# Optimization experiments

Hardware: AMD Instinct MI355X
Metric: run time of the kernel (lower is better)

Reference implementation:

```python
import jax, jax.numpy as jnp
import numpy as np

B, T, D = 64, 2048, 64
M_DIM = 8            # pthdv_m
N_GROUPS = 4         # out_dim // m^2 * 4
GD = D // N_GROUPS   # 16, per-group channel dim
OUT_DIM = 64
SE_HID = OUT_DIM // 16  # reduction ratio 16 -> 4


def expm(A):
    """Batched matrix exponential via fixed scaling-and-squaring + Taylor-12.
    A: (..., m, m) with modest norm (skew-symmetric from small weights)."""
    s = 6
    A = A * (1.0 / (2 ** s))
    eye = jnp.eye(A.shape[-1], dtype=A.dtype)
    term = jnp.broadcast_to(eye, A.shape)
    out = term
    for k in range(1, 13):
        term = jnp.matmul(term, A) / k
        out = out + term
    for _ in range(s):
        out = jnp.matmul(out, out)
    return out


def layernorm(x, g, b, eps=1e-5):
    mu = jnp.mean(x, axis=-1, keepdims=True)
    var = jnp.var(x, axis=-1, keepdims=True)
    return (x - mu) * jax.lax.rsqrt(var + eps) * g + b


def lin_interp(f, t_out):
    """F.interpolate(mode='linear', align_corners=False) along axis 1. f: (B,L,C)."""
    L = f.shape[1]
    pos = (jnp.arange(t_out, dtype=f.dtype) + 0.5) * (L / t_out) - 0.5
    pos = jnp.clip(pos, 0.0, L - 1.0)
    i0 = jnp.floor(pos).astype(jnp.int32)
    i1 = jnp.minimum(i0 + 1, L - 1)
    w = (pos - i0.astype(f.dtype))[None, :, None]
    return f[:, i0] * (1.0 - w) + f[:, i1] * w


def setup_inputs() -> dict:
    key = jax.random.key(0)
    ks = jax.random.split(key, 8)
    x = jax.random.normal(ks[0], (B, T, D), dtype=jnp.float32)
    mask = jnp.ones((B, T), dtype=jnp.float32)
    W_dev = jax.random.normal(ks[1], (N_GROUPS, GD, M_DIM, M_DIM), dtype=jnp.float32) * 0.1
    ln_gamma = jnp.ones((M_DIM * M_DIM,), dtype=jnp.float32)
    ln_beta = jnp.zeros((M_DIM * M_DIM,), dtype=jnp.float32)
    cf = N_GROUPS * M_DIM * M_DIM  # 256
    proj_w = jax.random.normal(ks[2], (cf, OUT_DIM), dtype=jnp.float32) / np.sqrt(cf)
    proj_b = jnp.zeros((OUT_DIM,), dtype=jnp.float32)
    se_w1 = jax.random.normal(ks[3], (OUT_DIM, SE_HID), dtype=jnp.float32) / np.sqrt(OUT_DIM)
    se_b1 = jnp.zeros((SE_HID,), dtype=jnp.float32)
    se_w2 = jax.random.normal(ks[4], (SE_HID, OUT_DIM), dtype=jnp.float32) / np.sqrt(SE_HID)
    se_b2 = jnp.zeros((OUT_DIM,), dtype=jnp.float32)
    return {"x": x, "mask": mask, "W_dev": W_dev, "ln_gamma": ln_gamma, "ln_beta": ln_beta,
            "proj_w": proj_w, "proj_b": proj_b, "se_w1": se_w1, "se_b1": se_b1,
            "se_w2": se_w2, "se_b2": se_b2}


def reference(x, mask, W_dev, ln_gamma, ln_beta, proj_w, proj_b, se_w1, se_b1, se_w2, se_b2):
    Bc, Tc, Dc = x.shape
    # skew-symmetric (so(m)) projection of raw dev weights: (G, gd, m, m)
    Wl = jnp.tril(W_dev, k=-1)
    S = Wl - jnp.swapaxes(Wl, -1, -2)
    # grouped increments: (B, T-1, G, gd), masked
    xg = x.reshape(Bc, Tc, N_GROUPS, GD)
    dX = (xg[:, 1:] - xg[:, :-1]) * mask[:, 1:, None, None]
    # project increments to Lie algebra: (B, T', G, m, m)
    Mlie = jnp.einsum('btgd,gdij->btgij', dX, S)
    E = expm(Mlie)                                   # path development per window (kernel=2)
    f = E.reshape(Bc, Tc - 1, N_GROUPS, M_DIM * M_DIM)
    f = layernorm(f, ln_gamma, ln_beta)              # shared LN over m^2, per group
    f = f.reshape(Bc, Tc - 1, N_GROUPS * M_DIM * M_DIM)
    f = f @ proj_w + proj_b                          # (B, T-1, out_dim)
    f = lin_interp(f, Tc)                            # back to length T (stride=1)
    h = x + f
    # Squeeze-and-Excitation with masked average pooling
    denom = jnp.sum(mask, axis=1, keepdims=True)     # (B,1)
    pooled = jnp.sum(h * mask[:, :, None], axis=1) / denom  # (B, D)
    s = jax.nn.sigmoid(jax.nn.gelu(pooled @ se_w1 + se_b1, approximate=False) @ se_w2 + se_b2)
    h = h * s[:, None, :]
    out = h + x                                      # res_con is Identity (in_dim==out_dim, stride==1)
    return (out, mask)
```

## Files before the change

kernel.cpp:

```cpp
#include <hip/hip_runtime.h>

#define B_   64
#define T_   2048
#define TM1  2047
#define D_   64

#define PID(i,j) ((i)*((i)-1)/2 + (j))

typedef __attribute__((ext_vector_type(8))) short bf16x8;
typedef __attribute__((ext_vector_type(4))) float f32x4;

__device__ __forceinline__ unsigned f2bf(float v) {
    unsigned u = __float_as_uint(v);
    u = (u + 0x7FFFu + ((u >> 16) & 1u)) >> 16;
    return u;
}
__device__ __forceinline__ float bf2f(unsigned s) {
    return __uint_as_float(s << 16);
}

__global__ void k_prep(const float* __restrict__ pw, unsigned short* __restrict__ pwB)
{
    int idx = blockIdx.x * 256 + threadIdx.x;
    int j  = idx & 7;
    int l  = (idx >> 3) & 63;
    int ks = (idx >> 9) & 7;
    int nt = idx >> 12;
    int k  = ks * 32 + ((l >> 4) << 3) + j;
    int o  = nt * 16 + (l & 15);
    pwB[idx] = (unsigned short)f2bf(pw[k * 64 + o]);
}

__global__ __launch_bounds__(256, 3) void k_expm_f2(
    const float* __restrict__ x, const float* __restrict__ mask,
    const float* __restrict__ Wd, const float* __restrict__ lng,
    const float* __restrict__ lnb, const unsigned short* __restrict__ pwB,
    const float* __restrict__ pb, unsigned short* __restrict__ fbf,
    float* __restrict__ pooled, float* __restrict__ denom)
{
    __shared__ __align__(16) unsigned char smem[32768];
    float* xT = (float*)smem;

    const int tid  = threadIdx.x;
    const int lane = tid & 63;
    const int wq   = __builtin_amdgcn_readfirstlane(tid >> 6);
    const int bl   = blockIdx.x >> 5;
    const int t0   = (blockIdx.x & 31) << 6;

    const float* xb = x + (size_t)bl * (T_ * D_);
    for (int idx = tid; idx < 65 * 64; idx += 256) {
        int r = idx >> 6, c = idx & 63;
        int tr = t0 + r;
        xT[c * 65 + r] = (tr < T_) ? xb[tr * 64 + c] : 0.f;
    }
    __syncthreads();

    const int t = t0 + lane;
    const bool valid = (t < TM1);
    const float* mrow = mask + bl * T_;
    const float mk = valid ? mrow[t + 1] : 0.f;

    {
        const int c  = tid & 63;
        const int rg = tid >> 6;
        float psum = 0.f;
        #pragma unroll
        for (int i = 0; i < 16; ++i) {
            int r = rg * 16 + i;
            psum = fmaf(xT[c * 65 + r], mrow[t0 + r], psum);
        }
        atomicAdd(&pooled[bl * 64 + c], psum);
        if (wq == 0) {
            float dv = mrow[t0 + lane];
            #pragma unroll
            for (int off = 32; off >= 1; off >>= 1) dv += __shfl_xor(dv, off);
            if (lane == 0) atomicAdd(&denom[bl], dv);
        }
    }

    float al[28];
    #pragma unroll
    for (int p = 0; p < 28; ++p) al[p] = 0.f;
    const float* Wg = Wd + wq * (16 * 64);
    #pragma unroll
    for (int d = 0; d < 16; ++d) {
        const float* col = &xT[(wq * 16 + d) * 65 + lane];
        float dxd = (col[1] - col[0]) * mk;
        const float* Wrow = Wg + d * 64;
        #pragma unroll
        for (int i = 1; i < 8; ++i)
            #pragma unroll
            for (int j = 0; j < i; ++j)
                al[PID(i, j)] = fmaf(dxd, Wrow[i * 8 + j], al[PID(i, j)]);
    }
    __syncthreads();

    #pragma unroll
    for (int p = 0; p < 28; ++p) al[p] *= 0.0625f;

    float R[64];
    #pragma unroll
    for (int i = 0; i < 8; ++i)
        #pragma unroll
        for (int j = 0; j < 8; ++j)
            R[i * 8 + j] = (i == j) ? 1.f : 0.f;
    for (int k = 6; k >= 1; --k) {
        float invk = 1.f / (float)k;
        #pragma unroll
        for (int j = 0; j < 8; ++j) {
            float tmp[8];
            #pragma unroll
            for (int i = 0; i < 8; ++i) tmp[i] = R[i * 8 + j];
            #pragma unroll
            for (int i = 0; i < 8; ++i) {
                float s = 0.f;
                #pragma unroll
                for (int kk = 0; kk < 8; ++kk) {
                    if (kk == i) continue;
                    float a = (i > kk) ? al[PID(i, kk)] : -al[PID(kk, i)];
                    s = fmaf(a, tmp[kk], s);
                }
                R[i * 8 + j] = ((i == j) ? 1.f : 0.f) + invk * s;
            }
        }
    }
    for (int sq = 0; sq < 4; ++sq) {
        float nw[64];
        #pragma unroll
        for (int i = 0; i < 8; ++i)
            #pragma unroll
            for (int j = 0; j < 8; ++j) {
                float s = 0.f;
                #pragma unroll
                for (int kk = 0; kk < 8; ++kk)
                    s = fmaf(R[i * 8 + kk], R[kk * 8 + j], s);
                nw[i * 8 + j] = s;
            }
        #pragma unroll
        for (int e = 0; e < 64; ++e) R[e] = nw[e];
    }

    float sum = 0.f, ssq = 0.f;
    #pragma unroll
    for (int e = 0; e < 64; ++e) { sum += R[e]; ssq = fmaf(R[e], R[e], ssq); }
    float mu   = sum * (1.f / 64.f);
    float var  = ssq * (1.f / 64.f) - mu * mu;
    float rstd = rsqrtf(var + 1e-5f);

    #pragma unroll
    for (int eq = 0; eq < 16; ++eq) {
        int e = eq * 4;
        float v0 = fmaf((R[e]   - mu) * rstd, lng[e],   lnb[e]);
        float v1 = fmaf((R[e+1] - mu) * rstd, lng[e+1], lnb[e+1]);
        float v2 = fmaf((R[e+2] - mu) * rstd, lng[e+2], lnb[e+2]);
        float v3 = fmaf((R[e+3] - mu) * rstd, lng[e+3], lnb[e+3]);
        uint2 pk = make_uint2(f2bf(v0) | (f2bf(v1) << 16), f2bf(v2) | (f2bf(v3) << 16));
        int slot = wq * 16 + eq;
        int sw = slot ^ ((lane & 7) << 1);
        *(uint2*)(smem + lane * 512 + sw * 8) = pk;
    }
    __syncthreads();

    f32x4 acc[4];
    #pragma unroll
    for (int nt = 0; nt < 4; ++nt) acc[nt] = (f32x4)(0.f);
    const int arow = wq * 16 + (lane & 15);
    #pragma unroll
    for (int ks = 0; ks < 8; ++ks) {
        int c = ks * 4 + (lane >> 4);
        bf16x8 a = *(const bf16x8*)(smem + arow * 512 + (c ^ (arow & 7)) * 16);
        #pragma unroll
        for (int nt = 0; nt < 4; ++nt) {
            bf16x8 bb = *(const bf16x8*)(pwB + (((nt * 8 + ks) * 64 + lane) << 3));
            acc[nt] = __builtin_amdgcn_mfma_f32_16x16x32_bf16(a, bb, acc[nt], 0, 0, 0);
        }
    }
    __syncthreads();

    unsigned short* fosh = (unsigned short*)smem;
    float bias[4];
    #pragma unroll
    for (int nt = 0; nt < 4; ++nt) bias[nt] = pb[nt * 16 + (lane & 15)];
    float pf[4] = {0.f, 0.f, 0.f, 0.f};
    #pragma unroll
    for (int r = 0; r < 4; ++r) {
        int pl = wq * 16 + ((lane >> 4) << 2) + r;
        int p  = t0 + pl;
        float g = 0.f;
        if (p < TM1) {
            float mp  = mrow[p];
            float mp1 = mrow[p + 1];
            float wlo = (p + 1.5f) * (1.f / 2048.f);
            float whi = 1.f - (p + 0.5f) * (1.f / 2048.f);
            if (p == 0)          g = mp + mp1 * wlo;
            else if (p == 2046)  g = mp * whi + mp1;
            else                 g = mp * whi + mp1 * wlo;
        }
        #pragma unroll
        for (int nt = 0; nt < 4; ++nt) {
            float fv = acc[nt][r] + bias[nt];
            pf[nt] = fmaf(g, fv, pf[nt]);
            fosh[pl * 64 + nt * 16 + (lane & 15)] = (unsigned short)f2bf(fv);
        }
    }
    #pragma unroll
    for (int nt = 0; nt < 4; ++nt) {
        pf[nt] += __shfl_xor(pf[nt], 16);
        pf[nt] += __shfl_xor(pf[nt], 32);
    }
    if (lane < 16) {
        #pragma unroll
        for (int nt = 0; nt < 4; ++nt)
            atomicAdd(&pooled[bl * 64 + nt * 16 + lane], pf[nt]);
    }
    __syncthreads();

    #pragma unroll
    for (int i = 0; i < 2; ++i) {
        int C = i * 256 + tid;
        int row = C >> 3, c = C & 7;
        int p = t0 + row;
        if (p < TM1) {
            uint4 vv = *(const uint4*)(smem + C * 16);
            *(uint4*)(fbf + ((size_t)bl * TM1 + p) * 64 + c * 8) = vv;
        }
    }
}

__global__ void k_se(const float* __restrict__ pooled, const float* __restrict__ denom,
                     const float* __restrict__ w1, const float* __restrict__ b1,
                     const float* __restrict__ w2, const float* __restrict__ b2,
                     float* __restrict__ s_out)
{
    __shared__ float pl[64];
    __shared__ float hid[4];
    const int b = blockIdx.x, o = threadIdx.x;
    float p = pooled[b * 64 + o] / denom[b];
    pl[o] = p;
    __syncthreads();
    if (o < 4) {
        float h = b1[o];
        for (int e = 0; e < 64; ++e) h = fmaf(pl[e], w1[e * 4 + o], h);
        hid[o] = 0.5f * h * (1.f + erff(h * 0.70710678118654752f));
    }
    __syncthreads();
    float sv = b2[o];
    #pragma unroll
    for (int hh = 0; hh < 4; ++hh) sv = fmaf(hid[hh], w2[hh * 64 + o], sv);
    s_out[b * 64 + o] = 1.f / (1.f + expf(-sv));
}

__global__ void k_apply(const float* __restrict__ x, const unsigned short* __restrict__ fbf,
                        const float* __restrict__ s, float* __restrict__ out)
{
    int gid = blockIdx.x * 256 + threadIdx.x;
    int o4 = (gid & 15) << 2;
    int t  = (gid >> 4) & 2047;
    int b  = gid >> 15;
    float pos = fminf(fmaxf((t + 0.5f) * (2047.f / 2048.f) - 0.5f, 0.f), 2046.f);
    int   i0  = (int)pos;
    float w   = pos - (float)i0;
    int   i1  = min(i0 + 1, 2046);
    const unsigned short* fb = fbf + (size_t)b * (TM1 * 64);
    uint2 u0 = *(const uint2*)(fb + i0 * 64 + o4);
    uint2 u1 = *(const uint2*)(fb + i1 * 64 + o4);
    size_t base = ((size_t)b * T_ + t) * 64 + o4;
    float4 xv = *(const float4*)(x + base);
    float4 sv = *(const float4*)(s + b * 64 + o4);
    float4 ov;
    float f00 = bf2f(u0.x & 0xffffu), f01 = bf2f(u0.x >> 16);
    float f02 = bf2f(u0.y & 0xffffu), f03 = bf2f(u0.y >> 16);
    float f10 = bf2f(u1.x & 0xffffu), f11 = bf2f(u1.x >> 16);
    float f12 = bf2f(u1.y & 0xffffu), f13 = bf2f(u1.y >> 16);
    ov.x = fmaf(xv.x + f00 * (1.f - w) + f10 * w, sv.x, xv.x);
    ov.y = fmaf(xv.y + f01 * (1.f - w) + f11 * w, sv.y, xv.y);
    ov.z = fmaf(xv.z + f02 * (1.f - w) + f12 * w, sv.z, xv.z);
    ov.w = fmaf(xv.w + f03 * (1.f - w) + f13 * w, sv.w, xv.w);
    *(float4*)(out + base) = ov;
}

extern "C" void kernel_launch(void* const* d_in, const int* in_sizes, int n_in,
                              void* d_out, int out_size, void* d_ws, size_t ws_size,
                              hipStream_t stream)
{
    const float* x    = (const float*)d_in[0];
    const float* mask = (const float*)d_in[1];
    const float* Wd   = (const float*)d_in[2];
    const float* lng  = (const float*)d_in[3];
    const float* lnb  = (const float*)d_in[4];
    const float* pw   = (const float*)d_in[5];
    const float* pb   = (const float*)d_in[6];
    const float* sw1  = (const float*)d_in[7];
    const float* sb1  = (const float*)d_in[8];
    const float* sw2  = (const float*)d_in[9];
    const float* sb2  = (const float*)d_in[10];

    float* out    = (float*)d_out;
    float* pooled = (float*)d_ws;
    float* denom  = pooled + 4096;
    float* s_ws   = denom + 64;
    unsigned short* pwB = (unsigned short*)(s_ws + 4096);
    unsigned short* fbf = pwB + 16384;

    hipMemsetAsync(pooled, 0, (4096 + 64) * sizeof(float), stream);

    hipLaunchKernelGGL(k_prep, dim3(64), dim3(256), 0, stream, pw, pwB);
    hipLaunchKernelGGL(k_expm_f2, dim3(2048), dim3(256), 0, stream,
                       x, mask, Wd, lng, lnb, pwB, pb, fbf, pooled, denom);
    hipLaunchKernelGGL(k_se, dim3(64), dim3(64), 0, stream,
                       pooled, denom, sw1, sb1, sw2, sb2, s_ws);
    hipLaunchKernelGGL(k_apply, dim3(8192), dim3(256), 0, stream,
                       x, fbf, s_ws, out);

    hipMemcpyAsync(out + (size_t)B_ * T_ * D_, mask,
                   (size_t)B_ * T_ * sizeof(float), hipMemcpyDeviceToDevice, stream);
}
```

Before: 222.3 us.

## Split each 8x8 expm across two lanes and fuse SE gate into apply

The expm kernel now assigns each timestep to a lane pair: each lane holds four columns of the matrix, Taylor terms are computed per column, and the squaring steps exchange columns via shuffles. Blocks cover 32 timesteps instead of 64, so twice as many blocks launch, and the launch-bounds occupancy hint is dropped. This is meant to cut per-thread register pressure from the 64-float matrix state and raise occupancy. The separate SE kernel is removed: every apply block recomputes the small gate MLP itself, trading redundant tiny work for one fewer launch.

```diff
diff --git a/kernel.cpp b/kernel.cpp
--- a/kernel.cpp
+++ b/kernel.cpp
@@ -31,61 +31,63 @@
     pwB[idx] = (unsigned short)f2bf(pw[k * 64 + o]);
 }
 
-__global__ __launch_bounds__(256, 3) void k_expm_f2(
+__global__ __launch_bounds__(256) void k_expm_s2(
     const float* __restrict__ x, const float* __restrict__ mask,
     const float* __restrict__ Wd, const float* __restrict__ lng,
     const float* __restrict__ lnb, const unsigned short* __restrict__ pwB,
     const float* __restrict__ pb, unsigned short* __restrict__ fbf,
     float* __restrict__ pooled, float* __restrict__ denom)
 {
-    __shared__ __align__(16) unsigned char smem[32768];
+    __shared__ __align__(16) unsigned char smem[20480];
     float* xT = (float*)smem;
 
     const int tid  = threadIdx.x;
     const int lane = tid & 63;
-    const int wq   = __builtin_amdgcn_readfirstlane(tid >> 6);
-    const int bl   = blockIdx.x >> 5;
-    const int t0   = (blockIdx.x & 31) << 6;
+    const int g    = __builtin_amdgcn_readfirstlane(tid >> 6);
+    const int tl   = lane >> 1;
+    const int h    = lane & 1;
+    const int bl   = blockIdx.x >> 6;
+    const int t0   = (blockIdx.x & 63) << 5;
 
     const float* xb = x + (size_t)bl * (T_ * D_);
-    for (int idx = tid; idx < 65 * 64; idx += 256) {
+    for (int idx = tid; idx < 33 * 64; idx += 256) {
         int r = idx >> 6, c = idx & 63;
         int tr = t0 + r;
-        xT[c * 65 + r] = (tr < T_) ? xb[tr * 64 + c] : 0.f;
-    }
-    __syncthreads();
-
-    const int t = t0 + lane;
-    const bool valid = (t < TM1);
+        xT[r * 65 + c] = (tr < T_) ? xb[tr * 64 + c] : 0.f;
+    }
+    __syncthreads();
+
     const float* mrow = mask + bl * T_;
-    const float mk = valid ? mrow[t + 1] : 0.f;
 
     {
-        const int c  = tid & 63;
-        const int rg = tid >> 6;
-        float psum = 0.f;
-        #pragma unroll
-        for (int i = 0; i < 16; ++i) {
-            int r = rg * 16 + i;
-            psum = fmaf(xT[c * 65 + r], mrow[t0 + r], psum);
-        }
-        atomicAdd(&pooled[bl * 64 + c], psum);
-        if (wq == 0) {
-            float dv = mrow[t0 + lane];
+        int c = tid & 63, rg = tid >> 6;
+        float ps = 0.f;
+        #pragma unroll
+        for (int i = 0; i < 8; ++i) {
+            int r = rg * 8 + i;
+            ps = fmaf(xT[r * 65 + c], mrow[t0 + r], ps);
+        }
+        atomicAdd(&pooled[bl * 64 + c], ps);
+        if (g == 0) {
+            float dv = (lane < 32) ? mrow[t0 + lane] : 0.f;
             #pragma unroll
             for (int off = 32; off >= 1; off >>= 1) dv += __shfl_xor(dv, off);
             if (lane == 0) atomicAdd(&denom[bl], dv);
         }
     }
 
+    const int t = t0 + tl;
+    const bool valid = (t < TM1);
+    const float mk = valid ? mrow[t + 1] : 0.f;
+
     float al[28];
     #pragma unroll
     for (int p = 0; p < 28; ++p) al[p] = 0.f;
-    const float* Wg = Wd + wq * (16 * 64);
-    #pragma unroll
-    for (int d = 0; d < 16; ++d) {
-        const float* col = &xT[(wq * 16 + d) * 65 + lane];
-        float dxd = (col[1] - col[0]) * mk;
+    const float* Wg = Wd + g * (16 * 64) + h * (8 * 64);
+    #pragma unroll
+    for (int d = 0; d < 8; ++d) {
+        int c = g * 16 + h * 8 + d;
+        float dxd = (xT[(tl + 1) * 65 + c] - xT[tl * 65 + c]) * mk;
         const float* Wrow = Wg + d * 64;
         #pragma unroll
         for (int i = 1; i < 8; ++i)
@@ -93,24 +95,24 @@
             for (int j = 0; j < i; ++j)
                 al[PID(i, j)] = fmaf(dxd, Wrow[i * 8 + j], al[PID(i, j)]);
     }
-    __syncthreads();
-
-    #pragma unroll
-    for (int p = 0; p < 28; ++p) al[p] *= 0.0625f;
-
-    float R[64];
-    #pragma unroll
-    for (int i = 0; i < 8; ++i)
-        #pragma unroll
-        for (int j = 0; j < 8; ++j)
-            R[i * 8 + j] = (i == j) ? 1.f : 0.f;
+    #pragma unroll
+    for (int p = 0; p < 28; ++p) al[p] = (al[p] + __shfl_xor(al[p], 1)) * 0.0625f;
+    __syncthreads();
+
+    float Rc[4][8];
+    #pragma unroll
+    for (int jj = 0; jj < 4; ++jj)
+        #pragma unroll
+        for (int i = 0; i < 8; ++i)
+            Rc[jj][i] = (i == 4 * h + jj) ? 1.f : 0.f;
     for (int k = 6; k >= 1; --k) {
         float invk = 1.f / (float)k;
         #pragma unroll
-        for (int j = 0; j < 8; ++j) {
+        for (int jj = 0; jj < 4; ++jj) {
+            int j = 4 * h + jj;
             float tmp[8];
             #pragma unroll
-            for (int i = 0; i < 8; ++i) tmp[i] = R[i * 8 + j];
+            for (int i = 0; i < 8; ++i) tmp[i] = Rc[jj][i];
             #pragma unroll
             for (int i = 0; i < 8; ++i) {
                 float s = 0.f;
@@ -120,143 +122,154 @@
                     float a = (i > kk) ? al[PID(i, kk)] : -al[PID(kk, i)];
                     s = fmaf(a, tmp[kk], s);
                 }
-                R[i * 8 + j] = ((i == j) ? 1.f : 0.f) + invk * s;
+                Rc[jj][i] = ((i == j) ? 1.f : 0.f) + invk * s;
             }
         }
     }
+
     for (int sq = 0; sq < 4; ++sq) {
-        float nw[64];
-        #pragma unroll
-        for (int i = 0; i < 8; ++i)
-            #pragma unroll
-            for (int j = 0; j < 8; ++j) {
-                float s = 0.f;
+        float acc2[4][8];
+        #pragma unroll
+        for (int jj = 0; jj < 4; ++jj)
+            #pragma unroll
+            for (int i = 0; i < 8; ++i) acc2[jj][i] = 0.f;
+        #pragma unroll
+        for (int kk = 0; kk < 8; ++kk) {
+            const int oj = kk & 3;
+            float colbuf[8];
+            #pragma unroll
+            for (int i = 0; i < 8; ++i) {
+                float other = __shfl_xor(Rc[oj][i], 1);
+                colbuf[i] = ((kk >> 2) == h) ? Rc[oj][i] : other;
+            }
+            #pragma unroll
+            for (int jj = 0; jj < 4; ++jj) {
+                float sc = Rc[jj][kk];
                 #pragma unroll
-                for (int kk = 0; kk < 8; ++kk)
-                    s = fmaf(R[i * 8 + kk], R[kk * 8 + j], s);
-                nw[i * 8 + j] = s;
+                for (int i = 0; i < 8; ++i)
+                    acc2[jj][i] = fmaf(colbuf[i], sc, acc2[jj][i]);
             }
-        #pragma unroll
-        for (int e = 0; e < 64; ++e) R[e] = nw[e];
+        }
+        #pragma unroll
+        for (int jj = 0; jj < 4; ++jj)
+            #pragma unroll
+            for (int i = 0; i < 8; ++i) Rc[jj][i] = acc2[jj][i];
     }
 
     float sum = 0.f, ssq = 0.f;
     #pragma unroll
-    for (int e = 0; e < 64; ++e) { sum += R[e]; ssq = fmaf(R[e], R[e], ssq); }
+    for (int jj = 0; jj < 4; ++jj)
+        #pragma unroll
+        for (int i = 0; i < 8; ++i) { float v = Rc[jj][i]; sum += v; ssq = fmaf(v, v, ssq); }
+    sum += __shfl_xor(sum, 1);
+    ssq += __shfl_xor(ssq, 1);
     float mu   = sum * (1.f / 64.f);
     float var  = ssq * (1.f / 64.f) - mu * mu;
     float rstd = rsqrtf(var + 1e-5f);
 
     #pragma unroll
-    for (int eq = 0; eq < 16; ++eq) {
-        int e = eq * 4;
-        float v0 = fmaf((R[e]   - mu) * rstd, lng[e],   lnb[e]);
-        float v1 = fmaf((R[e+1] - mu) * rstd, lng[e+1], lnb[e+1]);
-        float v2 = fmaf((R[e+2] - mu) * rstd, lng[e+2], lnb[e+2]);
-        float v3 = fmaf((R[e+3] - mu) * rstd, lng[e+3], lnb[e+3]);
+    for (int i = 0; i < 8; ++i) {
+        int e0 = i * 8 + 4 * h;
+        float v0 = fmaf((Rc[0][i] - mu) * rstd, lng[e0],     lnb[e0]);
+        float v1 = fmaf((Rc[1][i] - mu) * rstd, lng[e0 + 1], lnb[e0 + 1]);
+        float v2 = fmaf((Rc[2][i] - mu) * rstd, lng[e0 + 2], lnb[e0 + 2]);
+        float v3 = fmaf((Rc[3][i] - mu) * rstd, lng[e0 + 3], lnb[e0 + 3]);
         uint2 pk = make_uint2(f2bf(v0) | (f2bf(v1) << 16), f2bf(v2) | (f2bf(v3) << 16));
-        int slot = wq * 16 + eq;
-        int sw = slot ^ ((lane & 7) << 1);
-        *(uint2*)(smem + lane * 512 + sw * 8) = pk;
-    }
-    __syncthreads();
-
-    f32x4 acc[4];
-    #pragma unroll
-    for (int nt = 0; nt < 4; ++nt) acc[nt] = (f32x4)(0.f);
-    const int arow = wq * 16 + (lane & 15);
+        int g16 = (g * 8 + i) ^ (tl & 7);
+        *(uint2*)(smem + tl * 512 + g16 * 16 + h * 8) = pk;
+    }
+    __syncthreads();
+
+    const int rt = g & 1;
+    const int nh = g >> 1;
+    f32x4 acc[2];
+    acc[0] = (f32x4)(0.f); acc[1] = (f32x4)(0.f);
+    const int arow = rt * 16 + (lane & 15);
     #pragma unroll
     for (int ks = 0; ks < 8; ++ks) {
-        int c = ks * 4 + (lane >> 4);
-        bf16x8 a = *(const bf16x8*)(smem + arow * 512 + (c ^ (arow & 7)) * 16);
-        #pragma unroll
-        for (int nt = 0; nt < 4; ++nt) {
-            bf16x8 bb = *(const bf16x8*)(pwB + (((nt * 8 + ks) * 64 + lane) << 3));
-            acc[nt] = __builtin_amdgcn_mfma_f32_16x16x32_bf16(a, bb, acc[nt], 0, 0, 0);
-        }
-    }
-    __syncthreads();
-
-    unsigned short* fosh = (unsigned short*)smem;
-    float bias[4];
-    #pragma unroll
-    for (int nt = 0; nt < 4; ++nt) bias[nt] = pb[nt * 16 + (lane & 15)];
-    float pf[4] = {0.f, 0.f, 0.f, 0.f};
+        int c16 = ks * 4 + (lane >> 4);
+        bf16x8 a = *(const bf16x8*)(smem + arow * 512 + (c16 ^ (arow & 7)) * 16);
+        #pragma unroll
+        for (int ntl = 0; ntl < 2; ++ntl) {
+            int ntg = nh * 2 + ntl;
+            bf16x8 bb = *(const bf16x8*)(pwB + (((ntg * 8 + ks) * 64 + lane) << 3));
+            acc[ntl] = __builtin_amdgcn_mfma_f32_16x16x32_bf16(a, bb, acc[ntl], 0, 0, 0);
+        }
+    }
+
+    unsigned short* fosh = (unsigned short*)(smem + 16384);
+    float bias0 = pb[(nh * 2) * 16 + (lane & 15)];
+    float bias1 = pb[(nh * 2 + 1) * 16 + (lane & 15)];
+    float pf0 = 0.f, pf1 = 0.f;
     #pragma unroll
     for (int r = 0; r < 4; ++r) {
-        int pl = wq * 16 + ((lane >> 4) << 2) + r;
+        int pl = rt * 16 + ((lane >> 4) << 2) + r;
         int p  = t0 + pl;
-        float g = 0.f;
+        float gam = 0.f;
         if (p < TM1) {
             float mp  = mrow[p];
             float mp1 = mrow[p + 1];
             float wlo = (p + 1.5f) * (1.f / 2048.f);
             float whi = 1.f - (p + 0.5f) * (1.f / 2048.f);
-            if (p == 0)          g = mp + mp1 * wlo;
-            else if (p == 2046)  g = mp * whi + mp1;
-            else                 g = mp * whi + mp1 * wlo;
-        }
-        #pragma unroll
-        for (int nt = 0; nt < 4; ++nt) {
-            float fv = acc[nt][r] + bias[nt];
-            pf[nt] = fmaf(g, fv, pf[nt]);
-            fosh[pl * 64 + nt * 16 + (lane & 15)] = (unsigned short)f2bf(fv);
-        }
-    }
-    #pragma unroll
-    for (int nt = 0; nt < 4; ++nt) {
-        pf[nt] += __shfl_xor(pf[nt], 16);
-        pf[nt] += __shfl_xor(pf[nt], 32);
-    }
+            if (p == 0)          gam = mp + mp1 * wlo;
+            else if (p == 2046)  gam = mp * whi + mp1;
+            else                 gam = mp * whi + mp1 * wlo;
+        }
+        float fv0 = acc[0][r] + bias0;
+        float fv1 = acc[1][r] + bias1;
+        pf0 = fmaf(gam, fv0, pf0);
+        pf1 = fmaf(gam, fv1, pf1);
+        fosh[pl * 64 + (nh * 2) * 16 + (lane & 15)]     = (unsigned short)f2bf(fv0);
+        fosh[pl * 64 + (nh * 2 + 1) * 16 + (lane & 15)] = (unsigned short)f2bf(fv1);
+    }
+    pf0 += __shfl_xor(pf0, 16); pf0 += __shfl_xor(pf0, 32);
+    pf1 += __shfl_xor(pf1, 16); pf1 += __shfl_xor(pf1, 32);
     if (lane < 16) {
-        #pragma unroll
-        for (int nt = 0; nt < 4; ++nt)
-            atomicAdd(&pooled[bl * 64 + nt * 16 + lane], pf[nt]);
-    }
-    __syncthreads();
-
-    #pragma unroll
-    for (int i = 0; i < 2; ++i) {
-        int C = i * 256 + tid;
-        int row = C >> 3, c = C & 7;
+        atomicAdd(&pooled[bl * 64 + (nh * 2) * 16 + lane], pf0);
+        atomicAdd(&pooled[bl * 64 + (nh * 2 + 1) * 16 + lane], pf1);
+    }
+    __syncthreads();
+
+    {
+        int row = tid >> 3, c8 = tid & 7;
         int p = t0 + row;
         if (p < TM1) {
-            uint4 vv = *(const uint4*)(smem + C * 16);
-            *(uint4*)(fbf + ((size_t)bl * TM1 + p) * 64 + c * 8) = vv;
-        }
-    }
-}
-
-__global__ void k_se(const float* __restrict__ pooled, const float* __restrict__ denom,
-                     const float* __restrict__ w1, const float* __restrict__ b1,
-                     const float* __restrict__ w2, const float* __restrict__ b2,
-                     float* __restrict__ s_out)
+            uint4 vv = *(const uint4*)(fosh + row * 64 + c8 * 8);
+            *(uint4*)(fbf + ((size_t)bl * TM1 + p) * 64 + c8 * 8) = vv;
+        }
+    }
+}
+
+__global__ void k_apply2(const float* __restrict__ x, const unsigned short* __restrict__ fbf,
+                         const float* __restrict__ pooled, const float* __restrict__ denom,
+                         const float* __restrict__ w1, const float* __restrict__ b1,
+                         const float* __restrict__ w2, const float* __restrict__ b2,
+                         float* __restrict__ out)
 {
-    __shared__ float pl[64];
+    __shared__ float pl_[64];
     __shared__ float hid[4];
-    const int b = blockIdx.x, o = threadIdx.x;
-    float p = pooled[b * 64 + o] / denom[b];
-    pl[o] = p;
+    __shared__ __align__(16) float sgate[64];
+    const int b = blockIdx.x >> 7;
+    const int o = threadIdx.x;
+    if (o < 64) pl_[o] = pooled[b * 64 + o] / denom[b];
     __syncthreads();
     if (o < 4) {
-        float h = b1[o];
-        for (int e = 0; e < 64; ++e) h = fmaf(pl[e], w1[e * 4 + o], h);
-        hid[o] = 0.5f * h * (1.f + erff(h * 0.70710678118654752f));
-    }
-    __syncthreads();
-    float sv = b2[o];
-    #pragma unroll
-    for (int hh = 0; hh < 4; ++hh) sv = fmaf(hid[hh], w2[hh * 64 + o], sv);
-    s_out[b * 64 + o] = 1.f / (1.f + expf(-sv));
-}
-
-__global__ void k_apply(const float* __restrict__ x, const unsigned short* __restrict__ fbf,
-                        const float* __restrict__ s, float* __restrict__ out)
-{
-    int gid = blockIdx.x * 256 + threadIdx.x;
-    int o4 = (gid & 15) << 2;
-    int t  = (gid >> 4) & 2047;
-    int b  = gid >> 15;
+        float hv = b1[o];
+        for (int e = 0; e < 64; ++e) hv = fmaf(pl_[e], w1[e * 4 + o], hv);
+        hid[o] = 0.5f * hv * (1.f + erff(hv * 0.70710678118654752f));
+    }
+    __syncthreads();
+    if (o < 64) {
+        float sv = b2[o];
+        #pragma unroll
+        for (int hh = 0; hh < 4; ++hh) sv = fmaf(hid[hh], w2[hh * 64 + o], sv);
+        sgate[o] = 1.f / (1.f + expf(-sv));
+    }
+    __syncthreads();
+
+    const int o4   = (threadIdx.x & 15) << 2;
+    const int tloc = threadIdx.x >> 4;
+    const int t    = ((blockIdx.x & 127) << 4) + tloc;
     float pos = fminf(fmaxf((t + 0.5f) * (2047.f / 2048.f) - 0.5f, 0.f), 2046.f);
     int   i0  = (int)pos;
     float w   = pos - (float)i0;
@@ -266,7 +279,7 @@
     uint2 u1 = *(const uint2*)(fb + i1 * 64 + o4);
     size_t base = ((size_t)b * T_ + t) * 64 + o4;
     float4 xv = *(const float4*)(x + base);
-    float4 sv = *(const float4*)(s + b * 64 + o4);
+    float4 sv = *(const float4*)(&sgate[o4]);
     float4 ov;
     float f00 = bf2f(u0.x & 0xffffu), f01 = bf2f(u0.x >> 16);
     float f02 = bf2f(u0.y & 0xffffu), f03 = bf2f(u0.y >> 16);
@@ -298,19 +311,16 @@
     float* out    = (float*)d_out;
     float* pooled = (float*)d_ws;
     float* denom  = pooled + 4096;
-    float* s_ws   = denom + 64;
-    unsigned short* pwB = (unsigned short*)(s_ws + 4096);
+    unsigned short* pwB = (unsigned short*)(denom + 64);
     unsigned short* fbf = pwB + 16384;
 
     hipMemsetAsync(pooled, 0, (4096 + 64) * sizeof(float), stream);
 
     hipLaunchKernelGGL(k_prep, dim3(64), dim3(256), 0, stream, pw, pwB);
-    hipLaunchKernelGGL(k_expm_f2, dim3(2048), dim3(256), 0, stream,
+    hipLaunchKernelGGL(k_expm_s2, dim3(4096), dim3(256), 0, stream,
                        x, mask, Wd, lng, lnb, pwB, pb, fbf, pooled, denom);
-    hipLaunchKernelGGL(k_se, dim3(64), dim3(64), 0, stream,
-                       pooled, denom, sw1, sb1, sw2, sb2, s_ws);
-    hipLaunchKernelGGL(k_apply, dim3(8192), dim3(256), 0, stream,
-                       x, fbf, s_ws, out);
+    hipLaunchKernelGGL(k_apply2, dim3(8192), dim3(256), 0, stream,
+                       x, fbf, pooled, denom, sw1, sb1, sw2, sb2, out);
 
     hipMemcpyAsync(out + (size_t)B_ * T_ * D_, mask,
                    (size_t)B_ * T_ * sizeof(float), hipMemcpyDeviceToDevice, stream);
```

New measurement: 240.3 us. 1.08x slower.

## Use symmetric even/odd Taylor split for expm, fuse SE gate and mask copy

Applied to the files above, without the earlier changes.

The expm now scales by 1/8 instead of 1/16. It builds the symmetric powers A^2, A^4 and A^6 in packed upper-triangular form, then forms exp as an even-part polynomial plus A times an odd-part polynomial, needing only three squarings instead of four. This cuts FLOPs and register use in the per-thread matrix exponential, at the cost of a different truncation error. Separately, the memset moves into k_prep, the SE gate is computed per block inside the apply kernel with wave shuffles, and the mask copy is folded in, which removes three launches/ops.

```diff
diff --git a/kernel.cpp b/kernel.cpp
--- a/kernel.cpp
+++ b/kernel.cpp
@@ -6,6 +6,7 @@
 #define D_   64
 
 #define PID(i,j) ((i)*((i)-1)/2 + (j))
+#define UID(i,j) ((i)*8 + (j) - (i)*((i)+1)/2)
 
 typedef __attribute__((ext_vector_type(8))) short bf16x8;
 typedef __attribute__((ext_vector_type(4))) float f32x4;
@@ -19,7 +20,8 @@
     return __uint_as_float(s << 16);
 }
 
-__global__ void k_prep(const float* __restrict__ pw, unsigned short* __restrict__ pwB)
+__global__ void k_prep(const float* __restrict__ pw, unsigned short* __restrict__ pwB,
+                       float* __restrict__ pooled)
 {
     int idx = blockIdx.x * 256 + threadIdx.x;
     int j  = idx & 7;
@@ -29,9 +31,10 @@
     int k  = ks * 32 + ((l >> 4) << 3) + j;
     int o  = nt * 16 + (l & 15);
     pwB[idx] = (unsigned short)f2bf(pw[k * 64 + o]);
-}
-
-__global__ __launch_bounds__(256, 3) void k_expm_f2(
+    if (idx < 4160) pooled[idx] = 0.f;
+}
+
+__global__ __launch_bounds__(256, 3) void k_expm_f3(
     const float* __restrict__ x, const float* __restrict__ mask,
     const float* __restrict__ Wd, const float* __restrict__ lng,
     const float* __restrict__ lnb, const unsigned short* __restrict__ pwB,
@@ -96,35 +99,78 @@
     __syncthreads();
 
     #pragma unroll
-    for (int p = 0; p < 28; ++p) al[p] *= 0.0625f;
-
+    for (int p = 0; p < 28; ++p) al[p] *= 0.125f;
+
+    float Bu[36];
+    #pragma unroll
+    for (int i = 0; i < 8; ++i)
+        #pragma unroll
+        for (int j = i; j < 8; ++j) {
+            float s = 0.f;
+            #pragma unroll
+            for (int k = 0; k < 8; ++k) {
+                if (k == i || k == j) continue;
+                float aki = (k > i) ? al[PID(k, i)] : -al[PID(i, k)];
+                float akj = (k > j) ? al[PID(k, j)] : -al[PID(j, k)];
+                s = fmaf(aki, akj, s);
+            }
+            Bu[UID(i, j)] = -s;
+        }
+    float B2u[36];
+    #pragma unroll
+    for (int i = 0; i < 8; ++i)
+        #pragma unroll
+        for (int j = i; j < 8; ++j) {
+            float s = 0.f;
+            #pragma unroll
+            for (int k = 0; k < 8; ++k) {
+                int l1 = (i < k) ? i : k, h1 = (i < k) ? k : i;
+                int l2 = (k < j) ? k : j, h2 = (k < j) ? j : k;
+                s = fmaf(Bu[UID(l1, h1)], Bu[UID(l2, h2)], s);
+            }
+            B2u[UID(i, j)] = s;
+        }
+    float B3u[36];
+    #pragma unroll
+    for (int i = 0; i < 8; ++i)
+        #pragma unroll
+        for (int j = i; j < 8; ++j) {
+            float s = 0.f;
+            #pragma unroll
+            for (int k = 0; k < 8; ++k) {
+                int l1 = (i < k) ? i : k, h1 = (i < k) ? k : i;
+                int l2 = (k < j) ? k : j, h2 = (k < j) ? j : k;
+                s = fmaf(Bu[UID(l1, h1)], B2u[UID(l2, h2)], s);
+            }
+            B3u[UID(i, j)] = s;
+        }
+    #pragma unroll
+    for (int i = 0; i < 8; ++i)
+        #pragma unroll
+        for (int j = i; j < 8; ++j) {
+            int id = UID(i, j);
+            float b = Bu[id], b2 = B2u[id], b3 = B3u[id];
+            float idm = (i == j) ? 1.f : 0.f;
+            Bu[id]  = fmaf(b3, 1.f/720.f,  fmaf(b2, 1.f/24.f,  fmaf(b, 0.5f,     idm)));
+            B2u[id] = fmaf(b3, 1.f/5040.f, fmaf(b2, 1.f/120.f, fmaf(b, 1.f/6.f,  idm)));
+        }
     float R[64];
     #pragma unroll
     for (int i = 0; i < 8; ++i)
         #pragma unroll
-        for (int j = 0; j < 8; ++j)
-            R[i * 8 + j] = (i == j) ? 1.f : 0.f;
-    for (int k = 6; k >= 1; --k) {
-        float invk = 1.f / (float)k;
-        #pragma unroll
         for (int j = 0; j < 8; ++j) {
-            float tmp[8];
-            #pragma unroll
-            for (int i = 0; i < 8; ++i) tmp[i] = R[i * 8 + j];
-            #pragma unroll
-            for (int i = 0; i < 8; ++i) {
-                float s = 0.f;
-                #pragma unroll
-                for (int kk = 0; kk < 8; ++kk) {
-                    if (kk == i) continue;
-                    float a = (i > kk) ? al[PID(i, kk)] : -al[PID(kk, i)];
-                    s = fmaf(a, tmp[kk], s);
-                }
-                R[i * 8 + j] = ((i == j) ? 1.f : 0.f) + invk * s;
-            }
-        }
-    }
-    for (int sq = 0; sq < 4; ++sq) {
+            int lo = (i < j) ? i : j, hi = (i < j) ? j : i;
+            float s = Bu[UID(lo, hi)];
+            #pragma unroll
+            for (int k = 0; k < 8; ++k) {
+                if (k == i) continue;
+                float aik = (i > k) ? al[PID(i, k)] : -al[PID(k, i)];
+                int l2 = (k < j) ? k : j, h2 = (k < j) ? j : k;
+                s = fmaf(aik, B2u[UID(l2, h2)], s);
+            }
+            R[i * 8 + j] = s;
+        }
+    for (int sq = 0; sq < 3; ++sq) {
         float nw[64];
         #pragma unroll
         for (int i = 0; i < 8; ++i)
@@ -227,56 +273,72 @@
     }
 }
 
-__global__ void k_se(const float* __restrict__ pooled, const float* __restrict__ denom,
-                     const float* __restrict__ w1, const float* __restrict__ b1,
-                     const float* __restrict__ w2, const float* __restrict__ b2,
-                     float* __restrict__ s_out)
+__global__ void k_apply2(const float* __restrict__ x, const unsigned short* __restrict__ fbf,
+                         const float* __restrict__ pooled, const float* __restrict__ denom,
+                         const float* __restrict__ mask,
+                         const float* __restrict__ w1, const float* __restrict__ b1,
+                         const float* __restrict__ w2, const float* __restrict__ b2,
+                         float* __restrict__ out, float* __restrict__ out_mask)
 {
-    __shared__ float pl[64];
-    __shared__ float hid[4];
-    const int b = blockIdx.x, o = threadIdx.x;
-    float p = pooled[b * 64 + o] / denom[b];
-    pl[o] = p;
-    __syncthreads();
-    if (o < 4) {
-        float h = b1[o];
-        for (int e = 0; e < 64; ++e) h = fmaf(pl[e], w1[e * 4 + o], h);
-        hid[o] = 0.5f * h * (1.f + erff(h * 0.70710678118654752f));
-    }
-    __syncthreads();
-    float sv = b2[o];
-    #pragma unroll
-    for (int hh = 0; hh < 4; ++hh) sv = fmaf(hid[hh], w2[hh * 64 + o], sv);
-    s_out[b * 64 + o] = 1.f / (1.f + expf(-sv));
-}
-
-__global__ void k_apply(const float* __restrict__ x, const unsigned short* __restrict__ fbf,
-                        const float* __restrict__ s, float* __restrict__ out)
-{
-    int gid = blockIdx.x * 256 + threadIdx.x;
-    int o4 = (gid & 15) << 2;
-    int t  = (gid >> 4) & 2047;
-    int b  = gid >> 15;
-    float pos = fminf(fmaxf((t + 0.5f) * (2047.f / 2048.f) - 0.5f, 0.f), 2046.f);
-    int   i0  = (int)pos;
-    float w   = pos - (float)i0;
-    int   i1  = min(i0 + 1, 2046);
+    __shared__ __align__(16) float sgate[64];
+    const int b  = blockIdx.x >> 5;
+    const int t0 = (blockIdx.x & 31) << 6;
+    const int tid = threadIdx.x;
+
+    if (tid < 64) {
+        float p = pooled[b * 64 + tid] / denom[b];
+        float hp0 = p * w1[tid * 4 + 0];
+        float hp1 = p * w1[tid * 4 + 1];
+        float hp2 = p * w1[tid * 4 + 2];
+        float hp3 = p * w1[tid * 4 + 3];
+        #pragma unroll
+        for (int off = 32; off >= 1; off >>= 1) {
+            hp0 += __shfl_xor(hp0, off);
+            hp1 += __shfl_xor(hp1, off);
+            hp2 += __shfl_xor(hp2, off);
+            hp3 += __shfl_xor(hp3, off);
+        }
+        float h0 = hp0 + b1[0], h1 = hp1 + b1[1], h2 = hp2 + b1[2], h3 = hp3 + b1[3];
+        h0 = 0.5f * h0 * (1.f + erff(h0 * 0.70710678118654752f));
+        h1 = 0.5f * h1 * (1.f + erff(h1 * 0.70710678118654752f));
+        h2 = 0.5f * h2 * (1.f + erff(h2 * 0.70710678118654752f));
+        h3 = 0.5f * h3 * (1.f + erff(h3 * 0.70710678118654752f));
+        float sv = b2[tid];
+        sv = fmaf(h0, w2[0 * 64 + tid], sv);
+        sv = fmaf(h1, w2[1 * 64 + tid], sv);
+        sv = fmaf(h2, w2[2 * 64 + tid], sv);
+        sv = fmaf(h3, w2[3 * 64 + tid], sv);
+        sgate[tid] = 1.f / (1.f + expf(-sv));
+        out_mask[b * T_ + t0 + tid] = mask[b * T_ + t0 + tid];
+    }
+    __syncthreads();
+
     const unsigned short* fb = fbf + (size_t)b * (TM1 * 64);
-    uint2 u0 = *(const uint2*)(fb + i0 * 64 + o4);
-    uint2 u1 = *(const uint2*)(fb + i1 * 64 + o4);
-    size_t base = ((size_t)b * T_ + t) * 64 + o4;
-    float4 xv = *(const float4*)(x + base);
-    float4 sv = *(const float4*)(s + b * 64 + o4);
-    float4 ov;
-    float f00 = bf2f(u0.x & 0xffffu), f01 = bf2f(u0.x >> 16);
-    float f02 = bf2f(u0.y & 0xffffu), f03 = bf2f(u0.y >> 16);
-    float f10 = bf2f(u1.x & 0xffffu), f11 = bf2f(u1.x >> 16);
-    float f12 = bf2f(u1.y & 0xffffu), f13 = bf2f(u1.y >> 16);
-    ov.x = fmaf(xv.x + f00 * (1.f - w) + f10 * w, sv.x, xv.x);
-    ov.y = fmaf(xv.y + f01 * (1.f - w) + f11 * w, sv.y, xv.y);
-    ov.z = fmaf(xv.z + f02 * (1.f - w) + f12 * w, sv.z, xv.z);
-    ov.w = fmaf(xv.w + f03 * (1.f - w) + f13 * w, sv.w, xv.w);
-    *(float4*)(out + base) = ov;
+    #pragma unroll
+    for (int r = 0; r < 4; ++r) {
+        int u  = r * 256 + tid;
+        int t  = t0 + (u >> 4);
+        int o4 = (u & 15) << 2;
+        float pos = fminf(fmaxf((t + 0.5f) * (2047.f / 2048.f) - 0.5f, 0.f), 2046.f);
+        int   i0  = (int)pos;
+        float w   = pos - (float)i0;
+        int   i1  = min(i0 + 1, 2046);
+        uint2 u0 = *(const uint2*)(fb + i0 * 64 + o4);
+        uint2 u1 = *(const uint2*)(fb + i1 * 64 + o4);
+        size_t base = ((size_t)b * T_ + t) * 64 + o4;
+        float4 xv = *(const float4*)(x + base);
+        float4 sv = *(const float4*)(&sgate[o4]);
+        float4 ov;
+        float f00 = bf2f(u0.x & 0xffffu), f01 = bf2f(u0.x >> 16);
+        float f02 = bf2f(u0.y & 0xffffu), f03 = bf2f(u0.y >> 16);
+        float f10 = bf2f(u1.x & 0xffffu), f11 = bf2f(u1.x >> 16);
+        float f12 = bf2f(u1.y & 0xffffu), f13 = bf2f(u1.y >> 16);
+        ov.x = fmaf(xv.x + f00 * (1.f - w) + f10 * w, sv.x, xv.x);
+        ov.y = fmaf(xv.y + f01 * (1.f - w) + f11 * w, sv.y, xv.y);
+        ov.z = fmaf(xv.z + f02 * (1.f - w) + f12 * w, sv.z, xv.z);
+        ov.w = fmaf(xv.w + f03 * (1.f - w) + f13 * w, sv.w, xv.w);
+        *(float4*)(out + base) = ov;
+    }
 }
 
 extern "C" void kernel_launch(void* const* d_in, const int* in_sizes, int n_in,
@@ -295,23 +357,16 @@
     const float* sw2  = (const float*)d_in[9];
     const float* sb2  = (const float*)d_in[10];
 
-    float* out    = (float*)d_out;
+    float* out      = (float*)d_out;
+    float* out_mask = out + (size_t)B_ * T_ * D_;
     float* pooled = (float*)d_ws;
     float* denom  = pooled + 4096;
-    float* s_ws   = denom + 64;
-    unsigned short* pwB = (unsigned short*)(s_ws + 4096);
+    unsigned short* pwB = (unsigned short*)(denom + 64);
     unsigned short* fbf = pwB + 16384;
 
-    hipMemsetAsync(pooled, 0, (4096 + 64) * sizeof(float), stream);
-
-    hipLaunchKernelGGL(k_prep, dim3(64), dim3(256), 0, stream, pw, pwB);
-    hipLaunchKernelGGL(k_expm_f2, dim3(2048), dim3(256), 0, stream,
+    hipLaunchKernelGGL(k_prep, dim3(64), dim3(256), 0, stream, pw, pwB, pooled);
+    hipLaunchKernelGGL(k_expm_f3, dim3(2048), dim3(256), 0, stream,
                        x, mask, Wd, lng, lnb, pwB, pb, fbf, pooled, denom);
-    hipLaunchKernelGGL(k_se, dim3(64), dim3(64), 0, stream,
-                       pooled, denom, sw1, sb1, sw2, sb2, s_ws);
-    hipLaunchKernelGGL(k_apply, dim3(8192), dim3(256), 0, stream,
-                       x, fbf, s_ws, out);
-
-    hipMemcpyAsync(out + (size_t)B_ * T_ * D_, mask,
-                   (size_t)B_ * T_ * sizeof(float), hipMemcpyDeviceToDevice, stream);
-}
+    hipLaunchKernelGGL(k_apply2, dim3(2048), dim3(256), 0, stream,
+                       x, fbf, pooled, denom, mask, sw1, sb1, sw2, sb2, out, out_mask);
+}
```

New measurement: 197.5 us. 11.2% less time.
